# Kernel optimization log

Measured on AMD Instinct MI355X. Metric: run time of the kernel, lower is better.

Reference implementation:

```python
import jax, jax.numpy as jnp
import numpy as np
from itertools import combinations

F = 24                 # num_fields
VOCAB_PER_FIELD = 10000
D = 16                 # embed_dim
B = 2048               # batch
FIELD_DIMS = [VOCAB_PER_FIELD] * F
TOTAL_VOCAB = sum(FIELD_DIMS)
# FeaturesEmbedding/FeaturesLinear offsets: cumulative field dims
OFFSETS = np.concatenate(([0], np.cumsum(FIELD_DIMS)[:-1])).astype(np.int64)  # (F,)
PAIRS = np.array(list(combinations(range(F), 2)), dtype=np.int64)   # (276, 2)
TRIPS = np.array(list(combinations(range(F), 3)), dtype=np.int64)   # (2024, 3)


def setup_inputs() -> dict:
    key = jax.random.key(0)
    k0, k1, k2, k3, k4 = jax.random.split(key, 5)
    x = jax.random.randint(k0, (B, F), 0, VOCAB_PER_FIELD)
    embed_table = jax.random.normal(k1, (TOTAL_VOCAB, D), dtype=jnp.float32) * 0.01
    lin_weight = jax.random.normal(k2, (TOTAL_VOCAB, 1), dtype=jnp.float32) * 0.01
    lin_bias = jnp.zeros((1,), dtype=jnp.float32)
    genotype_2nd = jax.random.normal(k3, (PAIRS.shape[0], 1), dtype=jnp.float32)
    genotype_3rd = jax.random.normal(k4, (TRIPS.shape[0], 1), dtype=jnp.float32)
    return {
        "x": x,
        "embed_table": embed_table,
        "lin_weight": lin_weight,
        "lin_bias": lin_bias,
        "genotype_2nd": genotype_2nd,
        "genotype_3rd": genotype_3rd,
    }


def reference(x, embed_table, lin_weight, lin_bias, genotype_2nd, genotype_3rd):
    idx = x + jnp.asarray(OFFSETS)[None, :]            # (B, F) global ids
    emb = embed_table[idx]                             # (B, F, D)
    # genotype is detached in the original forward
    g2 = jax.lax.stop_gradient(genotype_2nd)[:, 0]     # (P,)
    g3 = jax.lax.stop_gradient(genotype_3rd)[:, 0]     # (T,)
    # 2nd-order gated interactions: sum_t sum_d g2[t] * e_i * e_j
    p = emb[:, PAIRS[:, 0]]                            # (B, P, D)
    q = emb[:, PAIRS[:, 1]]
    nasfm_2nd = jnp.einsum('bpd,bpd,p->b', p, q, g2)   # (B,)
    # 3rd-order gated interactions
    p1 = emb[:, TRIPS[:, 0]]                           # (B, T, D)
    q1 = emb[:, TRIPS[:, 1]]
    r1 = emb[:, TRIPS[:, 2]]
    nasfm_3rd = jnp.einsum('btd,btd,btd,t->b', p1, q1, r1, g3)  # (B,)
    # FeaturesLinear: sum of per-feature weights + bias
    linear = jnp.sum(lin_weight[idx][..., 0], axis=1) + lin_bias[0]  # (B,)
    return jax.nn.sigmoid(linear + nasfm_2nd + nasfm_3rd)
```

## Files before the change

### kernel.cpp

```cpp
#include <hip/hip_runtime.h>
#include <math.h>

#define F 24
#define D 16
#define BATCH 2048
#define NPAIR 276
#define NTRIP 2024
#define VOCAB 10000
#define NSLOT 18
#define SLOTF 28
#define SLABF (F * D + 8)

__host__ __device__ constexpr int pair_base(int i) { return i * 23 - i * (i - 1) / 2; }
__host__ __device__ constexpr int trip_base(int i) {
    return NTRIP - (24 - i) * (23 - i) * (22 - i) / 6;
}
__host__ __device__ constexpr int trip_idx(int i, int j, int k) {
    return trip_base(i) + (j - i - 1) * (46 - i - j) / 2 + (k - j - 1);
}
__host__ __device__ constexpr int PB(int c) { return (NPAIR * c) / 16; }

__global__ void repack_kernel(const float* __restrict__ g2,
                              const float* __restrict__ g3,
                              float* __restrict__ cw) {
    int s = blockIdx.x * blockDim.x + threadIdx.x;
    if (s >= 16 * NSLOT) return;
    int c = s / NSLOT, q = s - c * NSLOT;
    float* o = cw + s * SLOTF;
    for (int t = 0; t < SLOTF; ++t) o[t] = 0.f;
    int p = PB(c) + q;
    if (p < PB(c + 1)) {
        int i = 0;
        while (pair_base(i + 1) <= p) ++i;
        int j = i + 1 + (p - pair_base(i));
        o[0] = __int_as_float(i);
        o[1] = __int_as_float(j);
        o[2] = g2[p];
        if (j < 23) {
            int tb = trip_idx(i, j, j + 1);
            for (int k = j + 1; k < F; ++k) o[4 + k] = g3[tb + (k - j - 1)];
        }
    }
}

__global__ __launch_bounds__(1024, 4) void ctr_main(
    const int* __restrict__ x, const float* __restrict__ emb,
    const float* __restrict__ lw, const float* __restrict__ lb,
    const float* __restrict__ cw, float* __restrict__ out) {
    __shared__ float s_e[4 * SLABF];
    __shared__ int   s_idx[4 * F];
    __shared__ float s_lw[4 * F];
    __shared__ float s_part[4][16];

    const int tid = threadIdx.x;
    const int row0 = blockIdx.x * 4;

    if (tid < 4 * F) {
        int r = tid / F, f = tid - r * F;
        int idx = x[(row0 + r) * F + f] + f * VOCAB;
        s_idx[tid] = idx;
        s_lw[tid] = lw[idx];
    }
    __syncthreads();

    if (tid < 4 * F * 4) {
        int seg = tid >> 2, q = tid & 3;
        int r = seg / F, f = seg - r * F;
        float4 v = reinterpret_cast<const float4*>(emb)[s_idx[seg] * 4 + q];
        float* b = &s_e[r * SLABF + f * D + q * 4];
        b[0] = v.x; b[1] = v.y; b[2] = v.z; b[3] = v.w;
    }
    __syncthreads();

    const int d = tid & 15;
    const int r = (tid >> 4) & 3;
    const int w = __builtin_amdgcn_readfirstlane(tid >> 6);
    const float* se = &s_e[r * SLABF];

    float e[F];
#pragma unroll
    for (int f = 0; f < F; ++f) e[f] = se[f * D + d];

    const float4* cp = reinterpret_cast<const float4*>(cw) + w * (NSLOT * 7);
    float acc = 0.f;
#pragma unroll 2
    for (int s = 0; s < NSLOT; ++s) {
        float4 h  = cp[s * 7 + 0];
        float4 c0 = cp[s * 7 + 1], c1 = cp[s * 7 + 2], c2 = cp[s * 7 + 3];
        float4 c3 = cp[s * 7 + 4], c4 = cp[s * 7 + 5], c5 = cp[s * 7 + 6];
        int i = __float_as_int(h.x), j = __float_as_int(h.y);
        float ei = se[i * D + d];
        float ej = se[j * D + d];
        float ta = h.z, tb = 0.f;
        ta = fmaf(c0.x, e[0],  ta); tb = fmaf(c0.y, e[1],  tb);
        ta = fmaf(c0.z, e[2],  ta); tb = fmaf(c0.w, e[3],  tb);
        ta = fmaf(c1.x, e[4],  ta); tb = fmaf(c1.y, e[5],  tb);
        ta = fmaf(c1.z, e[6],  ta); tb = fmaf(c1.w, e[7],  tb);
        ta = fmaf(c2.x, e[8],  ta); tb = fmaf(c2.y, e[9],  tb);
        ta = fmaf(c2.z, e[10], ta); tb = fmaf(c2.w, e[11], tb);
        ta = fmaf(c3.x, e[12], ta); tb = fmaf(c3.y, e[13], tb);
        ta = fmaf(c3.z, e[14], ta); tb = fmaf(c3.w, e[15], tb);
        ta = fmaf(c4.x, e[16], ta); tb = fmaf(c4.y, e[17], tb);
        ta = fmaf(c4.z, e[18], ta); tb = fmaf(c4.w, e[19], tb);
        ta = fmaf(c5.x, e[20], ta); tb = fmaf(c5.y, e[21], tb);
        ta = fmaf(c5.z, e[22], ta); tb = fmaf(c5.w, e[23], tb);
        acc = fmaf(ei * ej, ta + tb, acc);
    }

#pragma unroll
    for (int m = 1; m < 16; m <<= 1) acc += __shfl_xor(acc, m, 64);
    if (d == 0) s_part[r][w] = acc;
    __syncthreads();

    if (tid < 64) {
        int rr = tid >> 4, c = tid & 15;
        float v = s_part[rr][c];
#pragma unroll
        for (int m = 1; m < 16; m <<= 1) v += __shfl_xor(v, m, 64);
        if (c == 0) {
            float lin = lb[0];
#pragma unroll
            for (int f = 0; f < F; ++f) lin += s_lw[rr * F + f];
            float z = v + lin;
            out[row0 + rr] = 1.f / (1.f + __expf(-z));
        }
    }
}

extern "C" void kernel_launch(void* const* d_in, const int* in_sizes, int n_in,
                              void* d_out, int out_size, void* d_ws, size_t ws_size,
                              hipStream_t stream) {
    const int*   x   = (const int*)d_in[0];
    const float* emb = (const float*)d_in[1];
    const float* lw  = (const float*)d_in[2];
    const float* lb  = (const float*)d_in[3];
    const float* g2  = (const float*)d_in[4];
    const float* g3  = (const float*)d_in[5];
    float* out = (float*)d_out;
    float* cw  = (float*)d_ws;

    hipLaunchKernelGGL(repack_kernel, dim3(2), dim3(256), 0, stream, g2, g3, cw);
    hipLaunchKernelGGL(ctr_main, dim3(BATCH / 4), dim3(1024), 0, stream,
                       x, emb, lw, lb, cw, out);
}
```

Measured before the change: 19.80 us.

## Process one batch row per 256-thread block with 16 pair chunks

```diff
diff --git a/kernel.cpp b/kernel.cpp
--- a/kernel.cpp
+++ b/kernel.cpp
@@ -7,9 +7,8 @@
 #define NPAIR 276
 #define NTRIP 2024
 #define VOCAB 10000
-#define NSLOT 18
+#define NSLOT_TOT 288
 #define SLOTF 28
-#define SLABF (F * D + 8)
 
 __host__ __device__ constexpr int pair_base(int i) { return i * 23 - i * (i - 1) / 2; }
 __host__ __device__ constexpr int trip_base(int i) {
@@ -18,24 +17,21 @@
 __host__ __device__ constexpr int trip_idx(int i, int j, int k) {
     return trip_base(i) + (j - i - 1) * (46 - i - j) / 2 + (k - j - 1);
 }
-__host__ __device__ constexpr int PB(int c) { return (NPAIR * c) / 16; }
 
 __global__ void repack_kernel(const float* __restrict__ g2,
                               const float* __restrict__ g3,
                               float* __restrict__ cw) {
     int s = blockIdx.x * blockDim.x + threadIdx.x;
-    if (s >= 16 * NSLOT) return;
-    int c = s / NSLOT, q = s - c * NSLOT;
+    if (s >= NSLOT_TOT) return;
     float* o = cw + s * SLOTF;
     for (int t = 0; t < SLOTF; ++t) o[t] = 0.f;
-    int p = PB(c) + q;
-    if (p < PB(c + 1)) {
+    if (s < NPAIR) {
         int i = 0;
-        while (pair_base(i + 1) <= p) ++i;
-        int j = i + 1 + (p - pair_base(i));
+        while (pair_base(i + 1) <= s) ++i;
+        int j = i + 1 + (s - pair_base(i));
         o[0] = __int_as_float(i);
         o[1] = __int_as_float(j);
-        o[2] = g2[p];
+        o[2] = g2[s];
         if (j < 23) {
             int tb = trip_idx(i, j, j + 1);
             for (int k = j + 1; k < F; ++k) o[4 + k] = g3[tb + (k - j - 1)];
@@ -43,48 +39,47 @@
     }
 }
 
-__global__ __launch_bounds__(1024, 4) void ctr_main(
+__global__ __launch_bounds__(256, 8) void ctr_main(
     const int* __restrict__ x, const float* __restrict__ emb,
     const float* __restrict__ lw, const float* __restrict__ lb,
     const float* __restrict__ cw, float* __restrict__ out) {
-    __shared__ float s_e[4 * SLABF];
-    __shared__ int   s_idx[4 * F];
-    __shared__ float s_lw[4 * F];
-    __shared__ float s_part[4][16];
+    __shared__ float s_e[F * D];
+    __shared__ int   s_idx[F];
+    __shared__ float s_lw[F];
+    __shared__ float s_part[16];
 
     const int tid = threadIdx.x;
-    const int row0 = blockIdx.x * 4;
+    const int row = blockIdx.x;
 
-    if (tid < 4 * F) {
-        int r = tid / F, f = tid - r * F;
-        int idx = x[(row0 + r) * F + f] + f * VOCAB;
+    if (tid < F) {
+        int idx = x[row * F + tid] + tid * VOCAB;
         s_idx[tid] = idx;
         s_lw[tid] = lw[idx];
     }
     __syncthreads();
 
-    if (tid < 4 * F * 4) {
-        int seg = tid >> 2, q = tid & 3;
-        int r = seg / F, f = seg - r * F;
-        float4 v = reinterpret_cast<const float4*>(emb)[s_idx[seg] * 4 + q];
-        float* b = &s_e[r * SLABF + f * D + q * 4];
+    if (tid < F * 4) {
+        int f = tid >> 2, q = tid & 3;
+        float4 v = reinterpret_cast<const float4*>(emb)[s_idx[f] * 4 + q];
+        float* b = &s_e[f * D + q * 4];
         b[0] = v.x; b[1] = v.y; b[2] = v.z; b[3] = v.w;
     }
     __syncthreads();
 
     const int d = tid & 15;
-    const int r = (tid >> 4) & 3;
-    const int w = __builtin_amdgcn_readfirstlane(tid >> 6);
-    const float* se = &s_e[r * SLABF];
+    const int sg = (tid >> 4) & 3;
+    const int w = tid >> 6;
+    const int chunk = w * 4 + sg;
+    const float* se = s_e;
 
     float e[F];
 #pragma unroll
     for (int f = 0; f < F; ++f) e[f] = se[f * D + d];
 
-    const float4* cp = reinterpret_cast<const float4*>(cw) + w * (NSLOT * 7);
+    const float4* cp = reinterpret_cast<const float4*>(cw) + chunk * (18 * 7);
     float acc = 0.f;
-#pragma unroll 2
-    for (int s = 0; s < NSLOT; ++s) {
+#pragma unroll 1
+    for (int s = 0; s < 18; ++s) {
         float4 h  = cp[s * 7 + 0];
         float4 c0 = cp[s * 7 + 1], c1 = cp[s * 7 + 2], c2 = cp[s * 7 + 3];
         float4 c3 = cp[s * 7 + 4], c4 = cp[s * 7 + 5], c5 = cp[s * 7 + 6];
@@ -109,20 +104,19 @@
 
 #pragma unroll
     for (int m = 1; m < 16; m <<= 1) acc += __shfl_xor(acc, m, 64);
-    if (d == 0) s_part[r][w] = acc;
+    if (d == 0) s_part[chunk] = acc;
     __syncthreads();
 
-    if (tid < 64) {
-        int rr = tid >> 4, c = tid & 15;
-        float v = s_part[rr][c];
+    if (tid < 16) {
+        float v = s_part[tid];
 #pragma unroll
         for (int m = 1; m < 16; m <<= 1) v += __shfl_xor(v, m, 64);
-        if (c == 0) {
+        if (tid == 0) {
             float lin = lb[0];
 #pragma unroll
-            for (int f = 0; f < F; ++f) lin += s_lw[rr * F + f];
+            for (int f = 0; f < F; ++f) lin += s_lw[f];
             float z = v + lin;
-            out[row0 + rr] = 1.f / (1.f + __expf(-z));
+            out[row] = 1.f / (1.f + __expf(-z));
         }
     }
 }
@@ -140,6 +134,6 @@
     float* cw  = (float*)d_ws;
 
     hipLaunchKernelGGL(repack_kernel, dim3(2), dim3(256), 0, stream, g2, g3, cw);
-    hipLaunchKernelGGL(ctr_main, dim3(BATCH / 4), dim3(1024), 0, stream,
+    hipLaunchKernelGGL(ctr_main, dim3(BATCH), dim3(256), 0, stream,
                        x, emb, lw, lb, cw, out);
 }
```

After: 41.26 us. +108.3%, slower.

## Split pair slots into long and short coefficient layouts to skip zero FMAs

Applied to the files above, without the earlier changes.

```diff
diff --git a/kernel.cpp b/kernel.cpp
--- a/kernel.cpp
+++ b/kernel.cpp
@@ -7,9 +7,11 @@
 #define NPAIR 276
 #define NTRIP 2024
 #define VOCAB 10000
-#define NSLOT 18
-#define SLOTF 28
-#define SLABF (F * D + 8)
+#define SLAB 392
+#define LONG_SLOTS 80
+#define SHORT_SLOTS 224
+#define LONG_F (LONG_SLOTS * 28)
+#define CW_FLOATS (LONG_F + SHORT_SLOTS * 16)
 
 __host__ __device__ constexpr int pair_base(int i) { return i * 23 - i * (i - 1) / 2; }
 __host__ __device__ constexpr int trip_base(int i) {
@@ -18,27 +20,29 @@
 __host__ __device__ constexpr int trip_idx(int i, int j, int k) {
     return trip_base(i) + (j - i - 1) * (46 - i - j) / 2 + (k - j - 1);
 }
-__host__ __device__ constexpr int PB(int c) { return (NPAIR * c) / 16; }
 
 __global__ void repack_kernel(const float* __restrict__ g2,
                               const float* __restrict__ g3,
                               float* __restrict__ cw) {
-    int s = blockIdx.x * blockDim.x + threadIdx.x;
-    if (s >= 16 * NSLOT) return;
-    int c = s / NSLOT, q = s - c * NSLOT;
-    float* o = cw + s * SLOTF;
-    for (int t = 0; t < SLOTF; ++t) o[t] = 0.f;
-    int p = PB(c) + q;
-    if (p < PB(c + 1)) {
+    const int tid = threadIdx.x;
+    for (int t = tid; t < CW_FLOATS; t += 512) cw[t] = 0.f;
+    __syncthreads();
+    if (tid < NPAIR) {
+        const int p = tid;
         int i = 0;
         while (pair_base(i + 1) <= p) ++i;
-        int j = i + 1 + (p - pair_base(i));
-        o[0] = __int_as_float(i);
-        o[1] = __int_as_float(j);
-        o[2] = g2[p];
-        if (j < 23) {
-            int tb = trip_idx(i, j, j + 1);
-            for (int k = j + 1; k < F; ++k) o[4 + k] = g3[tb + (k - j - 1)];
+        const int j = i + 1 + (p - pair_base(i));
+        if (j <= 11) {
+            const int rank = i * 11 - i * (i - 1) / 2 + (j - i - 1);
+            float* o = cw + rank * 28;
+            o[0] = __int_as_float(i); o[1] = __int_as_float(j); o[2] = g2[p];
+            for (int k = j + 1; k < F; ++k) o[4 + k] = g3[trip_idx(i, j, k)];
+        } else {
+            const int rank = (i <= 11) ? (12 * i + (j - 12))
+                                       : (144 + (35 - i) * (i - 12) / 2 + (j - i - 1));
+            float* o = cw + LONG_F + rank * 16;
+            o[0] = __int_as_float(i); o[1] = __int_as_float(j); o[2] = g2[p];
+            for (int k = j + 1; k < F; ++k) o[k - 10] = g3[trip_idx(i, j, k)];
         }
     }
 }
@@ -47,10 +51,10 @@
     const int* __restrict__ x, const float* __restrict__ emb,
     const float* __restrict__ lw, const float* __restrict__ lb,
     const float* __restrict__ cw, float* __restrict__ out) {
-    __shared__ float s_e[4 * SLABF];
+    __shared__ float s_e[4 * SLAB];
     __shared__ int   s_idx[4 * F];
     __shared__ float s_lw[4 * F];
-    __shared__ float s_part[4][16];
+    __shared__ float s_part[16][4];
 
     const int tid = threadIdx.x;
     const int row0 = blockIdx.x * 4;
@@ -67,7 +71,7 @@
         int seg = tid >> 2, q = tid & 3;
         int r = seg / F, f = seg - r * F;
         float4 v = reinterpret_cast<const float4*>(emb)[s_idx[seg] * 4 + q];
-        float* b = &s_e[r * SLABF + f * D + q * 4];
+        float* b = &s_e[r * SLAB + f * D + q * 4];
         b[0] = v.x; b[1] = v.y; b[2] = v.z; b[3] = v.w;
     }
     __syncthreads();
@@ -75,24 +79,24 @@
     const int d = tid & 15;
     const int r = (tid >> 4) & 3;
     const int w = __builtin_amdgcn_readfirstlane(tid >> 6);
-    const float* se = &s_e[r * SLABF];
+    const float* se = &s_e[r * SLAB];
 
     float e[F];
 #pragma unroll
     for (int f = 0; f < F; ++f) e[f] = se[f * D + d];
 
-    const float4* cp = reinterpret_cast<const float4*>(cw) + w * (NSLOT * 7);
     float acc = 0.f;
+
+    const float4* Lp = reinterpret_cast<const float4*>(cw) + w * (5 * 7);
 #pragma unroll 2
-    for (int s = 0; s < NSLOT; ++s) {
-        float4 h  = cp[s * 7 + 0];
-        float4 c0 = cp[s * 7 + 1], c1 = cp[s * 7 + 2], c2 = cp[s * 7 + 3];
-        float4 c3 = cp[s * 7 + 4], c4 = cp[s * 7 + 5], c5 = cp[s * 7 + 6];
+    for (int s = 0; s < 5; ++s) {
+        float4 h  = Lp[s * 7 + 0];
+        float4 c0 = Lp[s * 7 + 1], c1 = Lp[s * 7 + 2], c2 = Lp[s * 7 + 3];
+        float4 c3 = Lp[s * 7 + 4], c4 = Lp[s * 7 + 5], c5 = Lp[s * 7 + 6];
         int i = __float_as_int(h.x), j = __float_as_int(h.y);
         float ei = se[i * D + d];
         float ej = se[j * D + d];
         float ta = h.z, tb = 0.f;
-        ta = fmaf(c0.x, e[0],  ta); tb = fmaf(c0.y, e[1],  tb);
         ta = fmaf(c0.z, e[2],  ta); tb = fmaf(c0.w, e[3],  tb);
         ta = fmaf(c1.x, e[4],  ta); tb = fmaf(c1.y, e[5],  tb);
         ta = fmaf(c1.z, e[6],  ta); tb = fmaf(c1.w, e[7],  tb);
@@ -107,14 +111,32 @@
         acc = fmaf(ei * ej, ta + tb, acc);
     }
 
+    const float4* Sp = reinterpret_cast<const float4*>(cw) + (LONG_F / 4) + w * (14 * 4);
+#pragma unroll 2
+    for (int s = 0; s < 14; ++s) {
+        float4 h  = Sp[s * 4 + 0];
+        float4 k0 = Sp[s * 4 + 1], k1 = Sp[s * 4 + 2], k2 = Sp[s * 4 + 3];
+        int i = __float_as_int(h.x), j = __float_as_int(h.y);
+        float ei = se[i * D + d];
+        float ej = se[j * D + d];
+        float ta = h.z, tb = 0.f;
+        ta = fmaf(h.w,  e[13], ta);
+        tb = fmaf(k0.x, e[14], tb); ta = fmaf(k0.y, e[15], ta);
+        tb = fmaf(k0.z, e[16], tb); ta = fmaf(k0.w, e[17], ta);
+        tb = fmaf(k1.x, e[18], tb); ta = fmaf(k1.y, e[19], ta);
+        tb = fmaf(k1.z, e[20], tb); ta = fmaf(k1.w, e[21], ta);
+        tb = fmaf(k2.x, e[22], tb); ta = fmaf(k2.y, e[23], ta);
+        acc = fmaf(ei * ej, ta + tb, acc);
+    }
+
 #pragma unroll
     for (int m = 1; m < 16; m <<= 1) acc += __shfl_xor(acc, m, 64);
-    if (d == 0) s_part[r][w] = acc;
+    if (d == 0) s_part[w][r] = acc;
     __syncthreads();
 
     if (tid < 64) {
-        int rr = tid >> 4, c = tid & 15;
-        float v = s_part[rr][c];
+        const int rr = tid >> 4, c = tid & 15;
+        float v = s_part[c][rr];
 #pragma unroll
         for (int m = 1; m < 16; m <<= 1) v += __shfl_xor(v, m, 64);
         if (c == 0) {
@@ -139,7 +161,7 @@
     float* out = (float*)d_out;
     float* cw  = (float*)d_ws;
 
-    hipLaunchKernelGGL(repack_kernel, dim3(2), dim3(256), 0, stream, g2, g3, cw);
+    hipLaunchKernelGGL(repack_kernel, dim3(1), dim3(512), 0, stream, g2, g3, cw);
     hipLaunchKernelGGL(ctr_main, dim3(BATCH / 4), dim3(1024), 0, stream,
                        x, emb, lw, lb, cw, out);
 }
```

Measured after the change: 19.74 us. No clear change (-0.3%).
